# Kernel optimization log

Hardware: AMD Instinct MI355X
Metric: run time of the kernel (lower is better)

## Reference

```python
import jax, jax.numpy as jnp
import numpy as np
from jax import lax

D = 128        # input_size
N_ATOMS = 4096
N_RES = 512
N_CONV = 4
VOCAB = 116

def setup_inputs() -> dict:
    key = jax.random.key(0)
    ks = jax.random.split(key, 16)
    s = 1.0 / np.sqrt(D)
    inp = {
        "adjacency": jax.random.uniform(ks[0], (N_ATOMS, N_ATOMS), jnp.float32),
        "membership": jax.random.uniform(ks[1], (N_RES, N_ATOMS), jnp.float32),
        "emb": jax.random.normal(ks[2], (VOCAB, D), jnp.float32),
        "lin_w": jax.random.uniform(ks[3], (D, D), jnp.float32, -s, s),
        "lin_b": jax.random.uniform(ks[4], (D,), jnp.float32, -s, s),
        "w_ih": jax.random.uniform(ks[5], (3 * D, D), jnp.float32, -s, s),
        "w_hh": jax.random.uniform(ks[6], (3 * D, D), jnp.float32, -s, s),
        "b_ih": jax.random.uniform(ks[7], (3 * D,), jnp.float32, -s, s),
        "b_hh": jax.random.uniform(ks[8], (3 * D,), jnp.float32, -s, s),
        "c1w": jax.random.normal(ks[9], (15, D, 3, 3), jnp.float32) * 0.05,
        "c1b": jnp.zeros((15,), jnp.float32),
        "c2w": jax.random.normal(ks[10], (12, 15, 3, 3), jnp.float32) * 0.05,
        "c2b": jnp.zeros((12,), jnp.float32),
        "c3w": jax.random.normal(ks[11], (12, 12, 3, 3), jnp.float32) * 0.05,
        "c3b": jnp.zeros((12,), jnp.float32),
        "atoms": jax.random.randint(ks[12], (N_ATOMS,), 0, VOCAB, jnp.int32),
    }
    return inp

def _conv(x, w, b):
    y = lax.conv_general_dilated(x, w, (1, 1), 'SAME',
                                 dimension_numbers=('NCHW', 'OIHW', 'NCHW'))
    return y + b[None, :, None, None]

def _forward(adjacency, membership, emb, lin_w, lin_b, w_ih, w_hh, b_ih, b_hh,
             c1w, c1b, c2w, c2b, c3w, c3b, atoms):
    h = emb[atoms]  # [N_ATOMS, D]

    def step(h_prev, _):
        x_in = (adjacency @ h_prev) @ lin_w.T + lin_b
        gi = x_in @ w_ih.T + b_ih      # [N, 3D]
        gh = h_prev @ w_hh.T + b_hh    # [N, 3D]
        i_r, i_z, i_n = jnp.split(gi, 3, axis=1)
        h_r, h_z, h_n = jnp.split(gh, 3, axis=1)
        r = jax.nn.sigmoid(i_r + h_r)
        z = jax.nn.sigmoid(i_z + h_z)
        n = jnp.tanh(i_n + r * h_n)
        h_t = (1.0 - z) * n + z * h_prev
        return h_t, None

    h, _ = lax.scan(step, h, None, length=N_CONV)

    hf = membership @ h                          # [R, D]
    hf = hf[:, None, :]                          # [R, 1, D]
    hf = (hf + jnp.transpose(hf, (1, 0, 2))) / 2  # [R, R, D]
    hf = hf.reshape(1, D, N_RES, N_RES)          # faithful torch .view (reinterpret, no transpose)

    out = jax.nn.relu(_conv(hf, c1w, c1b))
    out = jax.nn.relu(_conv(out, c2w, c2b))
    out = _conv(out, c3w, c3b)[0]                # squeeze -> [12, R, R]
    out = jax.nn.sigmoid((out + jnp.transpose(out, (0, 2, 1))) / 2)
    return out

def reference(adjacency, membership, emb, lin_w, lin_b, w_ih, w_hh, b_ih, b_hh,
              c1w, c1b, c2w, c2b, c3w, c3b, atoms):
    return _forward(adjacency, membership, emb, lin_w, lin_b, w_ih, w_hh,
                    b_ih, b_hh, c1w, c1b, c2w, c2b, c3w, c3b, atoms)
```

## Files before the change

kernel.cpp:

```cpp
#include <hip/hip_runtime.h>
#include <stdint.h>

typedef float f32x4 __attribute__((ext_vector_type(4)));

__device__ __forceinline__ float sigm(float x){ return 1.f/(1.f + __expf(-x)); }

__global__ void k_gather(const float* __restrict__ emb, const int* __restrict__ atoms,
                         float* __restrict__ h){
  int gid = blockIdx.x*256 + threadIdx.x;
  int i = gid >> 7, k = gid & 127;
  h[gid] = emb[atoms[i]*128 + k];
}

__global__ void k_wc(const float* __restrict__ w_ih, const float* __restrict__ lin_w,
                     float* __restrict__ WcT){
  int idx = blockIdx.x*256 + threadIdx.x;
  int g = idx >> 7, e = idx & 127;
  float s = 0.f;
  for (int d = 0; d < 128; d++) s += w_ih[g*128+d]*lin_w[d*128+e];
  WcT[e*384 + g] = s;
}

__global__ void k_trT(const float* __restrict__ w_hh, float* __restrict__ WhhT){
  int idx = blockIdx.x*256 + threadIdx.x;
  int g = idx >> 7, e = idx & 127;
  WhhT[e*384 + g] = w_hh[g*128 + e];
}

__global__ void k_bc(const float* __restrict__ w_ih, const float* __restrict__ lin_b,
                     const float* __restrict__ b_ih, float* __restrict__ bc){
  int g = blockIdx.x*128 + threadIdx.x;
  if (g >= 384) return;
  float s = b_ih[g];
  for (int d = 0; d < 128; d++) s += w_ih[g*128+d]*lin_b[d];
  bc[g] = s;
}

__global__ __launch_bounds__(512) void k_gemm_nt(const float* __restrict__ A,
    const float* __restrict__ B, float* __restrict__ part,
    int M, int lda, int kchunk)
{
  __shared__ float As[2][32*132];
  __shared__ float Bs[2][32*132];

  const int tid = threadIdx.x;
  const int m0  = blockIdx.x * 128;
  const int k0  = blockIdx.y * kchunk;
  const int chunks = kchunk >> 5;

  const int ar = tid >> 2;
  const int ac = tid & 3;
  const int br = tid >> 4;
  const int bc = tid & 15;
  const int tn = tid & 31;
  const int tm = tid >> 5;

  f32x4 pa[2], pb[2];

  auto load_regs = [&](int c){
    const float* Ab = A + (size_t)(m0 + ar)*lda + k0 + c*32 + ac*4;
    pa[0] = *(const f32x4*)(Ab);
    pa[1] = *(const f32x4*)(Ab + 16);
    const float* Bb = B + (size_t)(k0 + c*32 + br)*128 + bc*8;
    pb[0] = *(const f32x4*)(Bb);
    pb[1] = *(const f32x4*)(Bb + 4);
  };
  auto write_lds = [&](int buf){
    #pragma unroll
    for (int j = 0; j < 4; j++){
      As[buf][(ac*4 + j)*132 + ar]      = pa[0][j];
      As[buf][(ac*4 + 16 + j)*132 + ar] = pa[1][j];
    }
    *(f32x4*)&Bs[buf][br*132 + bc*8]     = pb[0];
    *(f32x4*)&Bs[buf][br*132 + bc*8 + 4] = pb[1];
  };

  f32x4 acc[8];
  #pragma unroll
  for (int i = 0; i < 8; i++) acc[i] = (f32x4){0,0,0,0};

  load_regs(0);
  write_lds(0);
  if (chunks > 1) load_regs(1);
  __syncthreads();

  for (int c = 0; c < chunks; ++c){
    int cur = c & 1;
    if (c+1 < chunks) write_lds(cur^1);
    const float* Ap = &As[cur][tm*8];
    const float* Bp = &Bs[cur][tn*4];
    #pragma unroll 8
    for (int kk = 0; kk < 32; kk++){
      f32x4 a0 = *(const f32x4*)(Ap + kk*132);
      f32x4 a1 = *(const f32x4*)(Ap + kk*132 + 4);
      f32x4 b  = *(const f32x4*)(Bp + kk*132);
      acc[0] += a0[0]*b; acc[1] += a0[1]*b; acc[2] += a0[2]*b; acc[3] += a0[3]*b;
      acc[4] += a1[0]*b; acc[5] += a1[1]*b; acc[6] += a1[2]*b; acc[7] += a1[3]*b;
    }
    if (c+2 < chunks) load_regs(c+2);
    __syncthreads();
  }

  float* P = part + ((size_t)blockIdx.y*M + m0 + tm*8)*128 + tn*4;
  #pragma unroll
  for (int i = 0; i < 8; i++)
    *(f32x4*)(P + (size_t)i*128) = acc[i];
}

__global__ void k_reduce(const float* __restrict__ part, float* __restrict__ out,
                         int nsplit, int stride4, int n4){
  int i = blockIdx.x*256 + threadIdx.x;
  if (i >= n4) return;
  const f32x4* p = (const f32x4*)part;
  f32x4 s = p[i];
  for (int sp = 1; sp < nsplit; sp++) s += p[(size_t)sp*stride4 + i];
  ((f32x4*)out)[i] = s;
}

__global__ __launch_bounds__(256) void k_wgemm(const float* __restrict__ A0,
    const float* __restrict__ A1, const float* __restrict__ W0,
    const float* __restrict__ W1, float* __restrict__ C0, float* __restrict__ C1,
    int M)
{
  __shared__ float As[128*68];
  const int tid = threadIdx.x;
  const int m0 = blockIdx.x * 64;
  const int gsr = blockIdx.y;
  const bool first = gsr < 3;
  const int gs = first ? gsr : gsr - 3;
  const float* A = first ? A0 : A1;
  const float* W = first ? W0 : W1;
  float* C = first ? C0 : C1;

  for (int i4 = tid; i4 < 2048; i4 += 256){
    int r = i4 >> 5, c4 = (i4 & 31) * 4;
    f32x4 v = *(const f32x4*)(A + (size_t)(m0 + r)*128 + c4);
    As[(c4+0)*68 + r] = v[0];
    As[(c4+1)*68 + r] = v[1];
    As[(c4+2)*68 + r] = v[2];
    As[(c4+3)*68 + r] = v[3];
  }
  __syncthreads();

  const int tn = tid & 31, tm = tid >> 5;
  f32x4 acc[8];
  #pragma unroll
  for (int i = 0; i < 8; i++) acc[i] = (f32x4){0,0,0,0};
  const float* Ab = &As[tm*8];
  const float* Wp = W + gs*128 + tn*4;
  #pragma unroll 4
  for (int k = 0; k < 128; k++){
    f32x4 a0 = *(const f32x4*)(Ab + k*68);
    f32x4 a1 = *(const f32x4*)(Ab + k*68 + 4);
    f32x4 b  = *(const f32x4*)(Wp + (size_t)k*384);
    #pragma unroll
    for (int i = 0; i < 4; i++) acc[i]   += a0[i]*b;
    #pragma unroll
    for (int i = 0; i < 4; i++) acc[4+i] += a1[i]*b;
  }
  float* Cp = C + (size_t)(m0 + tm*8)*384 + gs*128 + tn*4;
  #pragma unroll
  for (int i = 0; i < 8; i++)
    *(f32x4*)(Cp + (size_t)i*384) = acc[i];
}

__global__ void k_gate(const float* __restrict__ gi, const float* __restrict__ gh,
                       const float* __restrict__ bc, const float* __restrict__ bhh,
                       const float* __restrict__ hprev, float* __restrict__ hnew){
  int gid = blockIdx.x*256 + threadIdx.x;
  int i = gid >> 7, e = gid & 127;
  const float* gir = gi + (size_t)i*384;
  const float* ghr = gh + (size_t)i*384;
  float r = sigm(gir[e]       + bc[e]       + ghr[e]       + bhh[e]);
  float z = sigm(gir[128+e]   + bc[128+e]   + ghr[128+e]   + bhh[128+e]);
  float n = tanhf(gir[256+e]  + bc[256+e]   + r*(ghr[256+e] + bhh[256+e]));
  hnew[gid] = (1.f - z)*n + z*hprev[gid];
}

__global__ void k_T(const float* __restrict__ c1w, const float* __restrict__ m,
                    float* __restrict__ T, float* __restrict__ ws1){
  int blk = blockIdx.x;
  int oc = blk / 9, dydx = blk - oc*9;
  int tid = threadIdx.x;
  int q = tid >> 7, k = tid & 127;
  float acc = 0.f, accw = 0.f;
  for (int c = 0; c < 128; c++){
    float wv = c1w[(oc*128 + c)*9 + dydx];
    acc  += wv * m[(4*c + q)*128 + k];
    accw += wv;
  }
  T[((size_t)blk*4 + q)*128 + k] = acc;
  if (tid == 0) ws1[blk] = accw;
}

__global__ __launch_bounds__(256) void k_conv1(const float* __restrict__ T,
    const float* __restrict__ ws1, const float* __restrict__ m,
    const float* __restrict__ b1, float* __restrict__ out1){
  int y = blockIdx.x >> 1;
  int x = ((blockIdx.x & 1) << 8) + threadIdx.x;
  float acc[15];
  #pragma unroll
  for (int oc = 0; oc < 15; oc++) acc[oc] = 0.f;
  #pragma unroll
  for (int dy = 0; dy < 3; dy++){
    int yy = y + dy - 1;
    if (yy < 0 || yy >= 512) continue;
    int q = yy >> 7;
    int jy = (yy & 127) * 4;
    #pragma unroll
    for (int dx = 0; dx < 3; dx++){
      int xx = x + dx - 1;
      if (xx < 0 || xx >= 512) continue;
      int k = xx & 127;
      int j = jy + (xx >> 7);
      float mv = m[j*128 + k];
      int dydx = dy*3 + dx;
      #pragma unroll
      for (int oc = 0; oc < 15; oc++)
        acc[oc] += T[((size_t)(oc*9 + dydx)*4 + q)*128 + k] + ws1[oc*9 + dydx] * mv;
    }
  }
  size_t o = (size_t)y*512 + x;
  #pragma unroll
  for (int oc = 0; oc < 15; oc++){
    float v = 0.5f*acc[oc] + b1[oc];
    out1[(size_t)oc*262144 + o] = v > 0.f ? v : 0.f;
  }
}

template<int IC, int OC, bool RELU>
__global__ __launch_bounds__(128) void k_conv(const float* __restrict__ in,
    const float* __restrict__ w, const float* __restrict__ bias, float* __restrict__ out)
{
  __shared__ float xin[IC*10*66];
  int x0 = blockIdx.x * 64, y0 = blockIdx.y * 8;
  int tid = threadIdx.x;
  for (int i = tid; i < IC*10*66; i += 128){
    int ic = i / 660;
    int rem = i - ic*660;
    int iy = rem / 66;
    int ix = rem - iy*66;
    int gy = y0 + iy - 1, gx = x0 + ix - 1;
    float v = 0.f;
    if ((unsigned)gy < 512u && (unsigned)gx < 512u)
      v = in[(size_t)ic*262144 + (size_t)gy*512 + gx];
    xin[i] = v;
  }
  __syncthreads();
  int tx = tid & 15, ty = tid >> 4;
  float acc[OC][4];
  #pragma unroll
  for (int oc = 0; oc < OC; oc++){
    float b = bias[oc];
    acc[oc][0] = b; acc[oc][1] = b; acc[oc][2] = b; acc[oc][3] = b;
  }
  for (int ic = 0; ic < IC; ic++){
    #pragma unroll
    for (int dy = 0; dy < 3; dy++){
      const float* row = &xin[ic*660 + (ty+dy)*66 + tx*4];
      float r[6];
      #pragma unroll
      for (int j = 0; j < 6; j++) r[j] = row[j];
      #pragma unroll
      for (int dx = 0; dx < 3; dx++){
        #pragma unroll
        for (int oc = 0; oc < OC; oc++){
          float wv = w[(oc*IC + ic)*9 + dy*3 + dx];
          #pragma unroll
          for (int px = 0; px < 4; px++)
            acc[oc][px] += wv * r[dx+px];
        }
      }
    }
  }
  size_t o = (size_t)(y0 + ty)*512 + x0 + tx*4;
  #pragma unroll
  for (int oc = 0; oc < OC; oc++){
    f32x4 v;
    #pragma unroll
    for (int px = 0; px < 4; px++){
      float t = acc[oc][px];
      v[px] = RELU ? fmaxf(t, 0.f) : t;
    }
    *(f32x4*)(out + (size_t)oc*262144 + o) = v;
  }
}

__global__ __launch_bounds__(256) void k_final(const float* __restrict__ o3, float* __restrict__ out){
  __shared__ float B[32*33];
  int c = blockIdx.z;
  int ty = blockIdx.y, tx = blockIdx.x;
  const float* base = o3 + (size_t)c*262144;
  int tid = threadIdx.x;
  {
    int rrow = tid >> 3, cc = (tid & 7) * 4;
    f32x4 v = *(const f32x4*)(base + (size_t)(tx*32 + rrow)*512 + ty*32 + cc);
    B[rrow*33 + cc + 0] = v[0];
    B[rrow*33 + cc + 1] = v[1];
    B[rrow*33 + cc + 2] = v[2];
    B[rrow*33 + cc + 3] = v[3];
  }
  __syncthreads();
  int i = tid >> 3, j0 = (tid & 7) * 4;
  f32x4 a = *(const f32x4*)(base + (size_t)(ty*32 + i)*512 + tx*32 + j0);
  f32x4 o;
  #pragma unroll
  for (int j = 0; j < 4; j++){
    float v = 0.5f*(a[j] + B[(j0+j)*33 + i]);
    o[j] = sigm(v);
  }
  *(f32x4*)(out + (size_t)c*262144 + (size_t)(ty*32 + i)*512 + tx*32 + j0) = o;
}

extern "C" void kernel_launch(void* const* d_in, const int* in_sizes, int n_in,
                              void* d_out, int out_size, void* d_ws, size_t ws_size,
                              hipStream_t stream) {
  (void)in_sizes; (void)n_in; (void)out_size;
  const float* adj   = (const float*)d_in[0];
  const float* mem   = (const float*)d_in[1];
  const float* emb   = (const float*)d_in[2];
  const float* lin_w = (const float*)d_in[3];
  const float* lin_b = (const float*)d_in[4];
  const float* w_ih  = (const float*)d_in[5];
  const float* w_hh  = (const float*)d_in[6];
  const float* b_ih  = (const float*)d_in[7];
  const float* b_hh  = (const float*)d_in[8];
  const float* c1w   = (const float*)d_in[9];
  const float* c1b   = (const float*)d_in[10];
  const float* c2w   = (const float*)d_in[11];
  const float* c2b   = (const float*)d_in[12];
  const float* c3w   = (const float*)d_in[13];
  const float* c3b   = (const float*)d_in[14];
  const int*   atoms = (const int*)d_in[15];
  char* ws = (char*)d_ws;

  const bool big = ws_size >= 40780800u;
  const int  NS  = big ? 16 : 8;
  const int  NSm = big ? 64 : 32;
  const size_t partB = (size_t)NS * 2097152u;

  float* part = (float*)(ws + 0);
  float* gi   = (float*)(ws + 0);
  float* gh   = (float*)(ws + 6291456);
  float* out1 = (float*)(ws + 0);
  float* out2 = (float*)(ws + 15728640);
  float* out3 = (float*)(ws + 0);
  float* ah   = (float*)(ws + partB);
  float* h0   = (float*)(ws + partB + 2097152);
  float* h1   = (float*)(ws + partB + 4194304);
  char*  sm   = ws + partB + 6291456;
  float* WcT  = (float*)(sm);
  float* WhhT = (float*)(sm + 196608);
  float* bc   = (float*)(sm + 393216);
  float* mbuf = (float*)(sm + 394752);
  float* Tbuf = (float*)(sm + 656896);
  float* ws1  = (float*)(sm + 933376);

  k_wc<<<192, 256, 0, stream>>>(w_ih, lin_w, WcT);
  k_trT<<<192, 256, 0, stream>>>(w_hh, WhhT);
  k_bc<<<3, 128, 0, stream>>>(w_ih, lin_b, b_ih, bc);
  k_gather<<<2048, 256, 0, stream>>>(emb, atoms, h0);

  float* hc = h0; float* hn = h1;
  for (int it = 0; it < 4; it++){
    k_gemm_nt<<<dim3(32, NS), 512, 0, stream>>>(adj, hc, part, 4096, 4096, 4096/NS);
    k_reduce<<<512, 256, 0, stream>>>(part, ah, NS, 131072, 131072);
    k_wgemm<<<dim3(64, 6), 256, 0, stream>>>(ah, hc, WcT, WhhT, gi, gh, 4096);
    k_gate<<<2048, 256, 0, stream>>>(gi, gh, bc, b_hh, hc, hn);
    float* t = hc; hc = hn; hn = t;
  }

  k_gemm_nt<<<dim3(4, NSm), 512, 0, stream>>>(mem, hc, part, 512, 4096, 4096/NSm);
  k_reduce<<<64, 256, 0, stream>>>(part, mbuf, NSm, 16384, 16384);
  k_T<<<135, 512, 0, stream>>>(c1w, mbuf, Tbuf, ws1);
  k_conv1<<<1024, 256, 0, stream>>>(Tbuf, ws1, mbuf, c1b, out1);
  k_conv<15,12,true><<<dim3(8,64), 128, 0, stream>>>(out1, c2w, c2b, out2);
  k_conv<12,12,false><<<dim3(8,64), 128, 0, stream>>>(out2, c3w, c3b, out3);
  k_final<<<dim3(16,16,12), 256, 0, stream>>>(out3, (float*)d_out);
}
```

Measured before the change: 507.7 us.

## Fuse GRU weight GEMMs with gate nonlinearity into a single kernel

Replaces the two-stage wgemm plus gate kernels with one kernel that stages both the aggregated input and previous hidden state in shared memory, computes the r, z and n gate GEMM columns for a 32-column slice, and applies the GRU update directly. This removes the round trip of the 4096x384 gi and gh intermediates through global memory and one launch per iteration. In exchange each thread computes only a 1x4 output per pass with scalar LDS reads, so arithmetic intensity per thread drops and the A tiles are reloaded by four column blocks.

```diff
diff --git a/kernel.cpp b/kernel.cpp
--- a/kernel.cpp
+++ b/kernel.cpp
@@ -117,64 +117,70 @@
   ((f32x4*)out)[i] = s;
 }
 
-__global__ __launch_bounds__(256) void k_wgemm(const float* __restrict__ A0,
-    const float* __restrict__ A1, const float* __restrict__ W0,
-    const float* __restrict__ W1, float* __restrict__ C0, float* __restrict__ C1,
-    int M)
+__global__ __launch_bounds__(512) void k_gruF(const float* __restrict__ ah,
+    const float* __restrict__ h, const float* __restrict__ WcT,
+    const float* __restrict__ WhhT, const float* __restrict__ bcv,
+    const float* __restrict__ bhh, float* __restrict__ hnew)
 {
-  __shared__ float As[128*68];
+  __shared__ float Aa[128*68];
+  __shared__ float Ah[128*68];
   const int tid = threadIdx.x;
   const int m0 = blockIdx.x * 64;
-  const int gsr = blockIdx.y;
-  const bool first = gsr < 3;
-  const int gs = first ? gsr : gsr - 3;
-  const float* A = first ? A0 : A1;
-  const float* W = first ? W0 : W1;
-  float* C = first ? C0 : C1;
-
-  for (int i4 = tid; i4 < 2048; i4 += 256){
+  const int c0 = blockIdx.y * 32;
+
+  for (int i4 = tid; i4 < 2048; i4 += 512){
     int r = i4 >> 5, c4 = (i4 & 31) * 4;
-    f32x4 v = *(const f32x4*)(A + (size_t)(m0 + r)*128 + c4);
-    As[(c4+0)*68 + r] = v[0];
-    As[(c4+1)*68 + r] = v[1];
-    As[(c4+2)*68 + r] = v[2];
-    As[(c4+3)*68 + r] = v[3];
+    f32x4 va = *(const f32x4*)(ah + (size_t)(m0 + r)*128 + c4);
+    f32x4 vh = *(const f32x4*)(h  + (size_t)(m0 + r)*128 + c4);
+    #pragma unroll
+    for (int j = 0; j < 4; j++){
+      Aa[(c4+j)*68 + r] = va[j];
+      Ah[(c4+j)*68 + r] = vh[j];
+    }
   }
   __syncthreads();
 
-  const int tn = tid & 31, tm = tid >> 5;
-  f32x4 acc[8];
-  #pragma unroll
-  for (int i = 0; i < 8; i++) acc[i] = (f32x4){0,0,0,0};
-  const float* Ab = &As[tm*8];
-  const float* Wp = W + gs*128 + tn*4;
-  #pragma unroll 4
-  for (int k = 0; k < 128; k++){
-    f32x4 a0 = *(const f32x4*)(Ab + k*68);
-    f32x4 a1 = *(const f32x4*)(Ab + k*68 + 4);
-    f32x4 b  = *(const f32x4*)(Wp + (size_t)k*384);
-    #pragma unroll
-    for (int i = 0; i < 4; i++) acc[i]   += a0[i]*b;
-    #pragma unroll
-    for (int i = 0; i < 4; i++) acc[4+i] += a1[i]*b;
-  }
-  float* Cp = C + (size_t)(m0 + tm*8)*384 + gs*128 + tn*4;
-  #pragma unroll
-  for (int i = 0; i < 8; i++)
-    *(f32x4*)(Cp + (size_t)i*384) = acc[i];
-}
-
-__global__ void k_gate(const float* __restrict__ gi, const float* __restrict__ gh,
-                       const float* __restrict__ bc, const float* __restrict__ bhh,
-                       const float* __restrict__ hprev, float* __restrict__ hnew){
-  int gid = blockIdx.x*256 + threadIdx.x;
-  int i = gid >> 7, e = gid & 127;
-  const float* gir = gi + (size_t)i*384;
-  const float* ghr = gh + (size_t)i*384;
-  float r = sigm(gir[e]       + bc[e]       + ghr[e]       + bhh[e]);
-  float z = sigm(gir[128+e]   + bc[128+e]   + ghr[128+e]   + bhh[128+e]);
-  float n = tanhf(gir[256+e]  + bc[256+e]   + r*(ghr[256+e] + bhh[256+e]));
-  hnew[gid] = (1.f - z)*n + z*hprev[gid];
+  const int tn = tid & 7;
+  const int tm = tid >> 3;
+  const int col = c0 + tn*4;
+
+  f32x4 A0, B0;
+  auto pass = [&](int s){
+    f32x4 accA = {0,0,0,0}, accB = {0,0,0,0};
+    const float* Wa = WcT  + s*128 + col;
+    const float* Wb = WhhT + s*128 + col;
+    const float* pa = &Aa[tm];
+    const float* ph = &Ah[tm];
+    #pragma unroll 8
+    for (int k = 0; k < 128; k++){
+      float xa = pa[k*68];
+      float xh = ph[k*68];
+      f32x4 ba = *(const f32x4*)(Wa + (size_t)k*384);
+      f32x4 bb = *(const f32x4*)(Wb + (size_t)k*384);
+      accA += xa*ba;
+      accB += xh*bb;
+    }
+    A0 = accA; B0 = accB;
+  };
+
+  f32x4 rr, zz;
+  pass(0);
+  #pragma unroll
+  for (int j = 0; j < 4; j++)
+    rr[j] = sigm(A0[j] + bcv[col+j] + B0[j] + bhh[col+j]);
+  pass(1);
+  #pragma unroll
+  for (int j = 0; j < 4; j++)
+    zz[j] = sigm(A0[j] + bcv[128+col+j] + B0[j] + bhh[128+col+j]);
+  pass(2);
+  f32x4 o;
+  #pragma unroll
+  for (int j = 0; j < 4; j++){
+    float n  = tanhf(A0[j] + bcv[256+col+j] + rr[j]*(B0[j] + bhh[256+col+j]));
+    float hp = Ah[(col+j)*68 + tm];
+    o[j] = (1.f - zz[j])*n + zz[j]*hp;
+  }
+  *(f32x4*)(hnew + (size_t)(m0 + tm)*128 + col) = o;
 }
 
 __global__ void k_T(const float* __restrict__ c1w, const float* __restrict__ m,
@@ -340,8 +346,6 @@
   const size_t partB = (size_t)NS * 2097152u;
 
   float* part = (float*)(ws + 0);
-  float* gi   = (float*)(ws + 0);
-  float* gh   = (float*)(ws + 6291456);
   float* out1 = (float*)(ws + 0);
   float* out2 = (float*)(ws + 15728640);
   float* out3 = (float*)(ws + 0);
@@ -365,8 +369,7 @@
   for (int it = 0; it < 4; it++){
     k_gemm_nt<<<dim3(32, NS), 512, 0, stream>>>(adj, hc, part, 4096, 4096, 4096/NS);
     k_reduce<<<512, 256, 0, stream>>>(part, ah, NS, 131072, 131072);
-    k_wgemm<<<dim3(64, 6), 256, 0, stream>>>(ah, hc, WcT, WhhT, gi, gh, 4096);
-    k_gate<<<2048, 256, 0, stream>>>(gi, gh, bc, b_hh, hc, hn);
+    k_gruF<<<dim3(64, 4), 512, 0, stream>>>(ah, hc, WcT, WhhT, bc, b_hh, hn);
     float* t = hc; hc = hn; hn = t;
   }
 
```

Measured after the change: 652.9 us. +28.6%, slower.
